# Performance work log

Measured on AMD Instinct MI355X. Metric: run time of the kernel, lower is better.

## Reference

```python
import jax, jax.numpy as jnp
import numpy as np

INPUT_SIZE = 2048
HIDDEN_SIZE = 4096
NUM_CLASSES = 1000
BATCH = 4096


def setup_inputs() -> dict:
    key = jax.random.key(0)
    kx, k1, k2, k3 = jax.random.split(key, 4)
    x = jax.random.normal(kx, (BATCH, INPUT_SIZE), dtype=jnp.float32)
    w1 = jax.random.normal(k1, (INPUT_SIZE, HIDDEN_SIZE), dtype=jnp.float32) * 0.01
    b1 = jnp.zeros((HIDDEN_SIZE,), dtype=jnp.float32)
    w2 = jax.random.normal(k2, (HIDDEN_SIZE, HIDDEN_SIZE), dtype=jnp.float32) * 0.01
    b2 = jnp.zeros((HIDDEN_SIZE,), dtype=jnp.float32)
    w3 = jax.random.normal(k3, (HIDDEN_SIZE, NUM_CLASSES), dtype=jnp.float32) * 0.01
    b3 = jnp.zeros((NUM_CLASSES,), dtype=jnp.float32)
    return {"x": x, "w1": w1, "b1": b1, "w2": w2, "b2": b2, "w3": w3, "b3": b3}


def reference(x, w1, b1, w2, b2, w3, b3):
    # fused GEMM + bias + ReLU, equivalent to the original Python double-loop matmul
    h1 = jax.nn.relu(x @ w1 + b1)    # [B, H]
    h2 = jax.nn.relu(h1 @ w2 + b2)   # [B, H]
    out = h2 @ w3 + b3               # [B, C]
    return out
```

## Files before the change

### kernel.cpp

```cpp
#include <hip/hip_runtime.h>
#include <hip/hip_bf16.h>

typedef __bf16 bf16x8 __attribute__((ext_vector_type(8)));
typedef __bf16 bf16x4 __attribute__((ext_vector_type(4)));
typedef float floatx4 __attribute__((ext_vector_type(4)));

#define B_    4096
#define IN_   2048
#define HID_  4096
#define NC_   1000
#define NCP_  1024

__device__ __forceinline__ void transpose_cvt_dev(const float* __restrict__ src,
                                                  __bf16* __restrict__ dst,
                                                  int R, int C, int bx, int by,
                                                  float* tile ) {
    const int r0 = bx * 64;
    const int c0 = by * 64;
    const int t  = threadIdx.x;
#pragma unroll
    for (int it = 0; it < 4; ++it) {
        int lin = it * 256 + t;
        int sr = lin >> 4, c4 = lin & 15;
        int cb = c0 + c4 * 4;
        const float* s = src + (size_t)(r0 + sr) * C;
        float4 v;
        if (cb + 3 < C) {
            v = *(const float4*)(s + cb);
        } else {
            v.x = (cb + 0 < C) ? s[cb + 0] : 0.f;
            v.y = (cb + 1 < C) ? s[cb + 1] : 0.f;
            v.z = (cb + 2 < C) ? s[cb + 2] : 0.f;
            v.w = (cb + 3 < C) ? s[cb + 3] : 0.f;
        }
        tile[(c4 * 4 + 0) * 65 + sr] = v.x;
        tile[(c4 * 4 + 1) * 65 + sr] = v.y;
        tile[(c4 * 4 + 2) * 65 + sr] = v.z;
        tile[(c4 * 4 + 3) * 65 + sr] = v.w;
    }
    __syncthreads();
#pragma unroll
    for (int it = 0; it < 4; ++it) {
        int lin = it * 256 + t;
        int dr = lin >> 4, q4 = lin & 15;
        bf16x4 o;
#pragma unroll
        for (int j = 0; j < 4; ++j) o[j] = (__bf16)tile[dr * 65 + q4 * 4 + j];
        *(bf16x4*)(dst + (size_t)(c0 + dr) * R + r0 + q4 * 4) = o;
    }
}

__global__ __launch_bounds__(256) void prep(const float* __restrict__ x,
                                            __bf16* __restrict__ xb,
                                            const float* __restrict__ w1,
                                            __bf16* __restrict__ w1t,
                                            const float* __restrict__ w2,
                                            __bf16* __restrict__ w2t,
                                            const float* __restrict__ w3,
                                            __bf16* __restrict__ w3t) {
    __shared__ float tile[64 * 65];
    const int b = blockIdx.x;
    if (b < 4096) {
        int i = (b * 256 + (int)threadIdx.x) * 8;
        float4 a = *(const float4*)(x + i);
        float4 c = *(const float4*)(x + i + 4);
        bf16x8 o;
        o[0] = (__bf16)a.x; o[1] = (__bf16)a.y; o[2] = (__bf16)a.z; o[3] = (__bf16)a.w;
        o[4] = (__bf16)c.x; o[5] = (__bf16)c.y; o[6] = (__bf16)c.z; o[7] = (__bf16)c.w;
        *(bf16x8*)(xb + i) = o;
    } else if (b < 6144) {
        int l = b - 4096;
        transpose_cvt_dev(w1, w1t, IN_, HID_, l & 31, l >> 5, tile);
    } else if (b < 10240) {
        int l = b - 6144;
        transpose_cvt_dev(w2, w2t, HID_, HID_, l & 63, l >> 6, tile);
    } else {
        int l = b - 10240;
        transpose_cvt_dev(w3, w3t, HID_, NC_, l & 63, l >> 6, tile);
    }
}

template <bool RELU, bool OUT_BF16>
__global__ __launch_bounds__(256, 2) void gemm_bt(const __bf16* __restrict__ A,
                                                  const __bf16* __restrict__ Bt,
                                                  const float* __restrict__ bias,
                                                  void* __restrict__ Cv,
                                                  int M, int K, int Nstore) {
    __shared__ __bf16 sA[128 * 64];
    __shared__ __bf16 sB[128 * 64];

    const int tid   = threadIdx.x;
    const int lane  = tid & 63;
    const int wave  = tid >> 6;
    const int wr    = wave >> 1;
    const int wc    = wave & 1;
    const int mBase = blockIdx.y * 128;
    const int nBase = blockIdx.x * 128;
    const int lr    = lane >> 4;
    const int lc    = lane & 15;

    floatx4 acc[4][4];
#pragma unroll
    for (int i = 0; i < 4; ++i)
#pragma unroll
        for (int j = 0; j < 4; ++j) acc[i][j] = (floatx4)0.f;

    for (int k0 = 0; k0 < K; k0 += 64) {
#pragma unroll
        for (int it = 0; it < 4; ++it) {
            int lin = it * 256 + tid;
            int r   = lin >> 3;
            int kc  = (lin & 7) ^ (r & 7);
            const __bf16* ga = A  + (size_t)(mBase + r) * K + k0 + kc * 8;
            const __bf16* gb = Bt + (size_t)(nBase + r) * K + k0 + kc * 8;
            __builtin_amdgcn_global_load_lds(
                (__attribute__((address_space(1))) void*)ga,
                (__attribute__((address_space(3))) void*)(sA + lin * 8), 16, 0, 0);
            __builtin_amdgcn_global_load_lds(
                (__attribute__((address_space(1))) void*)gb,
                (__attribute__((address_space(3))) void*)(sB + lin * 8), 16, 0, 0);
        }
        __builtin_amdgcn_s_waitcnt(0);
        __syncthreads();

#pragma unroll
        for (int kk = 0; kk < 2; ++kk) {
            const int sw = (kk * 4 + lr) ^ (lc & 7);
            bf16x8 af[4], bfr[4];
#pragma unroll
            for (int i = 0; i < 4; ++i)
                af[i] = *(const bf16x8*)(sA + (wr * 64 + i * 16 + lc) * 64 + sw * 8);
#pragma unroll
            for (int j = 0; j < 4; ++j)
                bfr[j] = *(const bf16x8*)(sB + (wc * 64 + j * 16 + lc) * 64 + sw * 8);
#pragma unroll
            for (int i = 0; i < 4; ++i)
#pragma unroll
                for (int j = 0; j < 4; ++j)
                    acc[i][j] = __builtin_amdgcn_mfma_f32_16x16x32_bf16(af[i], bfr[j], acc[i][j], 0, 0, 0);
        }
        __syncthreads();
    }

#pragma unroll
    for (int j = 0; j < 4; ++j) {
        int col = nBase + wc * 64 + j * 16 + lc;
        if (col < Nstore) {
            float bv = bias[col];
#pragma unroll
            for (int i = 0; i < 4; ++i) {
                int rowb = mBase + wr * 64 + i * 16 + lr * 4;
#pragma unroll
                for (int r = 0; r < 4; ++r) {
                    float v = acc[i][j][r] + bv;
                    if (RELU) v = fmaxf(v, 0.f);
                    if (OUT_BF16)
                        ((__bf16*)Cv)[(size_t)(rowb + r) * Nstore + col] = (__bf16)v;
                    else
                        ((float*)Cv)[(size_t)(rowb + r) * Nstore + col] = v;
                }
            }
        }
    }
}

__global__ __launch_bounds__(256, 2) void gemm_sk(const __bf16* __restrict__ A,
                                                  const __bf16* __restrict__ Bt,
                                                  float* __restrict__ P,
                                                  int M, int KH, int Ktot) {
    __shared__ __bf16 sA[128 * 64];
    __shared__ __bf16 sB[128 * 64];

    const int tid   = threadIdx.x;
    const int lane  = tid & 63;
    const int wave  = tid >> 6;
    const int wr    = wave >> 1;
    const int wc    = wave & 1;
    const int mBase = blockIdx.y * 128;
    const int nBase = blockIdx.x * 128;
    const int z     = blockIdx.z;
    const int kOff  = z * KH;
    const int lr    = lane >> 4;
    const int lc    = lane & 15;

    floatx4 acc[4][4];
#pragma unroll
    for (int i = 0; i < 4; ++i)
#pragma unroll
        for (int j = 0; j < 4; ++j) acc[i][j] = (floatx4)0.f;

    for (int k0 = kOff; k0 < kOff + KH; k0 += 64) {
#pragma unroll
        for (int it = 0; it < 4; ++it) {
            int lin = it * 256 + tid;
            int r   = lin >> 3;
            int kc  = (lin & 7) ^ (r & 7);
            const __bf16* ga = A  + (size_t)(mBase + r) * Ktot + k0 + kc * 8;
            const __bf16* gb = Bt + (size_t)(nBase + r) * Ktot + k0 + kc * 8;
            __builtin_amdgcn_global_load_lds(
                (__attribute__((address_space(1))) void*)ga,
                (__attribute__((address_space(3))) void*)(sA + lin * 8), 16, 0, 0);
            __builtin_amdgcn_global_load_lds(
                (__attribute__((address_space(1))) void*)gb,
                (__attribute__((address_space(3))) void*)(sB + lin * 8), 16, 0, 0);
        }
        __builtin_amdgcn_s_waitcnt(0);
        __syncthreads();

#pragma unroll
        for (int kk = 0; kk < 2; ++kk) {
            const int sw = (kk * 4 + lr) ^ (lc & 7);
            bf16x8 af[4], bfr[4];
#pragma unroll
            for (int i = 0; i < 4; ++i)
                af[i] = *(const bf16x8*)(sA + (wr * 64 + i * 16 + lc) * 64 + sw * 8);
#pragma unroll
            for (int j = 0; j < 4; ++j)
                bfr[j] = *(const bf16x8*)(sB + (wc * 64 + j * 16 + lc) * 64 + sw * 8);
#pragma unroll
            for (int i = 0; i < 4; ++i)
#pragma unroll
                for (int j = 0; j < 4; ++j)
                    acc[i][j] = __builtin_amdgcn_mfma_f32_16x16x32_bf16(af[i], bfr[j], acc[i][j], 0, 0, 0);
        }
        __syncthreads();
    }

    float* Pz = P + (size_t)z * M * NCP_;
#pragma unroll
    for (int j = 0; j < 4; ++j) {
        int col = nBase + wc * 64 + j * 16 + lc;
#pragma unroll
        for (int i = 0; i < 4; ++i) {
            int rowb = mBase + wr * 64 + i * 16 + lr * 4;
#pragma unroll
            for (int r = 0; r < 4; ++r)
                Pz[(size_t)(rowb + r) * NCP_ + col] = acc[i][j][r];
        }
    }
}

__global__ __launch_bounds__(256) void reduce_bias(const float* __restrict__ P,
                                                   const float* __restrict__ b3,
                                                   float* __restrict__ out) {
    int c = blockIdx.x * 256 + threadIdx.x;
    int m = blockIdx.y;
    if (c < NC_)
        out[(size_t)m * NC_ + c] =
            P[(size_t)m * NCP_ + c] + P[(size_t)(B_ + m) * NCP_ + c] + b3[c];
}

extern "C" void kernel_launch(void* const* d_in, const int* in_sizes, int n_in,
                              void* d_out, int out_size, void* d_ws, size_t ws_size,
                              hipStream_t stream) {
    const float* x  = (const float*)d_in[0];
    const float* w1 = (const float*)d_in[1];
    const float* b1 = (const float*)d_in[2];
    const float* w2 = (const float*)d_in[3];
    const float* b2 = (const float*)d_in[4];
    const float* w3 = (const float*)d_in[5];
    const float* b3 = (const float*)d_in[6];
    float* out = (float*)d_out;

    char* ws = (char*)d_ws;
    __bf16* xb  = (__bf16*)(ws);
    __bf16* w1t = (__bf16*)(ws + (16u << 20));
    __bf16* w2t = (__bf16*)(ws + (32u << 20));
    __bf16* w3t = (__bf16*)(ws + (64u << 20));
    __bf16* h1  = (__bf16*)(ws + (72u << 20));
    __bf16* h2  = (__bf16*)(ws);
    float*  P   = (float*)(ws + (72u << 20));

    prep<<<11264, 256, 0, stream>>>(x, xb, w1, w1t, w2, w2t, w3, w3t);

    gemm_bt<true, true><<<dim3(HID_ / 128, B_ / 128), 256, 0, stream>>>(
        xb, w1t, b1, h1, B_, IN_, HID_);
    gemm_bt<true, true><<<dim3(HID_ / 128, B_ / 128), 256, 0, stream>>>(
        h1, w2t, b2, h2, B_, HID_, HID_);

    gemm_sk<<<dim3(NCP_ / 128, B_ / 128, 2), 256, 0, stream>>>(
        h2, w3t, P, B_, HID_ / 2, HID_);
    reduce_bias<<<dim3(NCP_ / 256, B_), 256, 0, stream>>>(P, b3, out);
}
```

Measured before the change: 428.3 us.

## Overlap w2/w3 transpose-convert with first GEMM in one fused launch

Splits the prep kernel so only x and w1 conversion run before GEMM1, then launches GEMM1 together with the w2 and w3 transpose-to-bf16 blocks in a single grid. The aim is for the memory-bound weight transposes to run alongside the compute-bound first GEMM instead of serially. The transpose output store is also widened from 4 to 8 bf16 per thread. The risk is that GEMM1 is slowed by sharing CUs and bandwidth with the transpose blocks, and that the shared-memory union could limit occupancy.

After: 423.0 us. No clear change (-1.3%).

```diff
diff --git a/kernel.cpp b/kernel.cpp
--- a/kernel.cpp
+++ b/kernel.cpp
@@ -40,62 +40,31 @@
     }
     __syncthreads();
 #pragma unroll
-    for (int it = 0; it < 4; ++it) {
+    for (int it = 0; it < 2; ++it) {
         int lin = it * 256 + t;
-        int dr = lin >> 4, q4 = lin & 15;
-        bf16x4 o;
-#pragma unroll
-        for (int j = 0; j < 4; ++j) o[j] = (__bf16)tile[dr * 65 + q4 * 4 + j];
-        *(bf16x4*)(dst + (size_t)(c0 + dr) * R + r0 + q4 * 4) = o;
-    }
-}
-
-__global__ __launch_bounds__(256) void prep(const float* __restrict__ x,
-                                            __bf16* __restrict__ xb,
-                                            const float* __restrict__ w1,
-                                            __bf16* __restrict__ w1t,
-                                            const float* __restrict__ w2,
-                                            __bf16* __restrict__ w2t,
-                                            const float* __restrict__ w3,
-                                            __bf16* __restrict__ w3t) {
-    __shared__ float tile[64 * 65];
-    const int b = blockIdx.x;
-    if (b < 4096) {
-        int i = (b * 256 + (int)threadIdx.x) * 8;
-        float4 a = *(const float4*)(x + i);
-        float4 c = *(const float4*)(x + i + 4);
+        int dr = lin >> 3, q8 = lin & 7;
         bf16x8 o;
-        o[0] = (__bf16)a.x; o[1] = (__bf16)a.y; o[2] = (__bf16)a.z; o[3] = (__bf16)a.w;
-        o[4] = (__bf16)c.x; o[5] = (__bf16)c.y; o[6] = (__bf16)c.z; o[7] = (__bf16)c.w;
-        *(bf16x8*)(xb + i) = o;
-    } else if (b < 6144) {
-        int l = b - 4096;
-        transpose_cvt_dev(w1, w1t, IN_, HID_, l & 31, l >> 5, tile);
-    } else if (b < 10240) {
-        int l = b - 6144;
-        transpose_cvt_dev(w2, w2t, HID_, HID_, l & 63, l >> 6, tile);
-    } else {
-        int l = b - 10240;
-        transpose_cvt_dev(w3, w3t, HID_, NC_, l & 63, l >> 6, tile);
+#pragma unroll
+        for (int j = 0; j < 8; ++j) o[j] = (__bf16)tile[dr * 65 + q8 * 8 + j];
+        *(bf16x8*)(dst + (size_t)(c0 + dr) * R + r0 + q8 * 8) = o;
     }
 }
 
 template <bool RELU, bool OUT_BF16>
-__global__ __launch_bounds__(256, 2) void gemm_bt(const __bf16* __restrict__ A,
-                                                  const __bf16* __restrict__ Bt,
-                                                  const float* __restrict__ bias,
-                                                  void* __restrict__ Cv,
-                                                  int M, int K, int Nstore) {
-    __shared__ __bf16 sA[128 * 64];
-    __shared__ __bf16 sB[128 * 64];
-
+__device__ __forceinline__ void gemm_core(const __bf16* __restrict__ A,
+                                          const __bf16* __restrict__ Bt,
+                                          const float* __restrict__ bias,
+                                          void* __restrict__ Cv,
+                                          int M, int K, int Nstore,
+                                          int bx, int by,
+                                          __bf16* sA, __bf16* sB) {
     const int tid   = threadIdx.x;
     const int lane  = tid & 63;
     const int wave  = tid >> 6;
     const int wr    = wave >> 1;
     const int wc    = wave & 1;
-    const int mBase = blockIdx.y * 128;
-    const int nBase = blockIdx.x * 128;
+    const int mBase = by * 128;
+    const int nBase = bx * 128;
     const int lr    = lane >> 4;
     const int lc    = lane & 15;
 
@@ -164,6 +133,61 @@
     }
 }
 
+__global__ __launch_bounds__(256) void prep1(const float* __restrict__ x,
+                                             __bf16* __restrict__ xb,
+                                             const float* __restrict__ w1,
+                                             __bf16* __restrict__ w1t) {
+    __shared__ float tile[64 * 65];
+    const int b = blockIdx.x;
+    if (b < 4096) {
+        int i = (b * 256 + (int)threadIdx.x) * 8;
+        float4 a = *(const float4*)(x + i);
+        float4 c = *(const float4*)(x + i + 4);
+        bf16x8 o;
+        o[0] = (__bf16)a.x; o[1] = (__bf16)a.y; o[2] = (__bf16)a.z; o[3] = (__bf16)a.w;
+        o[4] = (__bf16)c.x; o[5] = (__bf16)c.y; o[6] = (__bf16)c.z; o[7] = (__bf16)c.w;
+        *(bf16x8*)(xb + i) = o;
+    } else {
+        int l = b - 4096;
+        transpose_cvt_dev(w1, w1t, IN_, HID_, l & 31, l >> 5, tile);
+    }
+}
+
+__global__ __launch_bounds__(256, 2) void gemm1_fused(const __bf16* __restrict__ xb,
+                                                      const __bf16* __restrict__ w1t,
+                                                      const float* __restrict__ b1,
+                                                      __bf16* __restrict__ h1,
+                                                      const float* __restrict__ w2,
+                                                      __bf16* __restrict__ w2t,
+                                                      const float* __restrict__ w3,
+                                                      __bf16* __restrict__ w3t) {
+    __shared__ float smem[8192];
+    const int b = blockIdx.x;
+    if (b < 1024) {
+        __bf16* sA = (__bf16*)smem;
+        __bf16* sB = sA + 128 * 64;
+        gemm_core<true, true>(xb, w1t, b1, h1, B_, IN_, HID_, b & 31, b >> 5, sA, sB);
+    } else if (b < 5120) {
+        int l = b - 1024;
+        transpose_cvt_dev(w2, w2t, HID_, HID_, l & 63, l >> 6, smem);
+    } else {
+        int l = b - 5120;
+        transpose_cvt_dev(w3, w3t, HID_, NC_, l & 63, l >> 6, smem);
+    }
+}
+
+template <bool RELU, bool OUT_BF16>
+__global__ __launch_bounds__(256, 2) void gemm_bt(const __bf16* __restrict__ A,
+                                                  const __bf16* __restrict__ Bt,
+                                                  const float* __restrict__ bias,
+                                                  void* __restrict__ Cv,
+                                                  int M, int K, int Nstore) {
+    __shared__ __bf16 sA[128 * 64];
+    __shared__ __bf16 sB[128 * 64];
+    gemm_core<RELU, OUT_BF16>(A, Bt, bias, Cv, M, K, Nstore,
+                              blockIdx.x, blockIdx.y, sA, sB);
+}
+
 __global__ __launch_bounds__(256, 2) void gemm_sk(const __bf16* __restrict__ A,
                                                   const __bf16* __restrict__ Bt,
                                                   float* __restrict__ P,
@@ -271,10 +295,10 @@
     __bf16* h2  = (__bf16*)(ws);
     float*  P   = (float*)(ws + (72u << 20));
 
-    prep<<<11264, 256, 0, stream>>>(x, xb, w1, w1t, w2, w2t, w3, w3t);
-
-    gemm_bt<true, true><<<dim3(HID_ / 128, B_ / 128), 256, 0, stream>>>(
-        xb, w1t, b1, h1, B_, IN_, HID_);
+    prep1<<<6144, 256, 0, stream>>>(x, xb, w1, w1t);
+
+    gemm1_fused<<<6144, 256, 0, stream>>>(xb, w1t, b1, h1, w2, w2t, w3, w3t);
+
     gemm_bt<true, true><<<dim3(HID_ / 128, B_ / 128), 256, 0, stream>>>(
         h1, w2t, b2, h2, B_, HID_, HID_);
 
```
